# Kernel tuning notes

Measured on AMD Instinct MI355X. Metric: run time of the kernel, lower is better.

The kernel has to match this reference:

```python
import jax, jax.numpy as jnp
import numpy as np

B, N, D, H = 4, 2048, 1024, 16
HD = D // H
SCALE = D ** -0.5  # NOTE: original scales by dimension**-0.5 (not head_dim**-0.5)


def setup_inputs() -> dict:
    key = jax.random.key(0)
    k1, k2, k3 = jax.random.split(key, 3)
    x = jax.random.normal(k1, (B, N, D), dtype=jnp.float32)
    w_qkv = jax.random.normal(k2, (D, 3 * D), dtype=jnp.float32) * (D ** -0.5)
    w_proj = jax.random.normal(k3, (D, D), dtype=jnp.float32) * (D ** -0.5)
    b_proj = jnp.zeros((D,), dtype=jnp.float32)
    return {"x": x, "w_qkv": w_qkv, "w_proj": w_proj, "b_proj": b_proj}


def reference(x, w_qkv, w_proj, b_proj):
    # qkv projection: [B,N,3D] -> split into q,k,v each [B,H,N,HD]
    qkv = x @ w_qkv
    qkv = qkv.reshape(B, N, 3, H, HD).transpose(2, 0, 3, 1, 4)  # [3,B,H,N,HD]
    q, k, v = qkv[0], qkv[1], qkv[2]
    scores = jnp.einsum('bhid,bhjd->bhij', q, k) * SCALE
    attn = jax.nn.softmax(scores, axis=-1)
    out = jnp.einsum('bhij,bhjd->bhid', attn, v)  # [B,H,N,HD]
    out = out.transpose(0, 2, 1, 3).reshape(B, N, D)
    return out @ w_proj + b_proj
```

## Files before the change

### kernel.cpp

```cpp
#include <hip/hip_runtime.h>
#include <stdint.h>

#define Bdim 4
#define Nseq 2048
#define Dmod 1024
#define Hn   16
#define HD   64
#define SCALE 0.03125f
#define L2E   1.44269504089f

typedef __attribute__((ext_vector_type(8))) short short8;
typedef __attribute__((ext_vector_type(8))) unsigned short ushort8;
typedef __attribute__((ext_vector_type(4))) float f32x4;
typedef __attribute__((ext_vector_type(16))) float f32x16;

typedef __attribute__((address_space(3))) uint32_t lds_u32;
typedef __attribute__((address_space(1))) const uint32_t glob_u32;

static __device__ __forceinline__ void gload_lds16(const unsigned short* g, unsigned short* l) {
    __builtin_amdgcn_global_load_lds((glob_u32*)(const void*)g, (lds_u32*)(void*)l, 16, 0, 0);
}

static __device__ __forceinline__ unsigned short f2bf(float f) {
    union { float f; uint32_t u; } v; v.f = f;
    uint32_t r = (v.u + 0x7FFFu + ((v.u >> 16) & 1u)) >> 16;
    return (unsigned short)r;
}

__global__ __launch_bounds__(256) void cast_x_kernel(const float* __restrict__ in,
                                                     unsigned short* __restrict__ out, int n4) {
    int i = blockIdx.x * blockDim.x + threadIdx.x;
    int stride = gridDim.x * blockDim.x;
    for (; i < n4; i += stride) {
        float4 v = reinterpret_cast<const float4*>(in)[i];
        ushort4 o;
        o.x = f2bf(v.x); o.y = f2bf(v.y); o.z = f2bf(v.z); o.w = f2bf(v.w);
        reinterpret_cast<ushort4*>(out)[i] = o;
    }
}

__global__ void transpose_cast_kernel(const float* __restrict__ in,
                                      unsigned short* __restrict__ out, int R, int C) {
    __shared__ unsigned short t[32][33];
    int c0 = blockIdx.x * 32, r0 = blockIdx.y * 32;
    int tx = threadIdx.x, ty = threadIdx.y;
#pragma unroll
    for (int i = 0; i < 4; ++i)
        t[ty + i*8][tx] = f2bf(in[(size_t)(r0 + ty + i*8) * C + c0 + tx]);
    __syncthreads();
#pragma unroll
    for (int i = 0; i < 4; ++i)
        out[(size_t)(c0 + ty + i*8) * R + r0 + tx] = t[tx][ty + i*8];
}

template<bool OUT_BF16, bool BIAS, bool VSPLIT>
__global__ __launch_bounds__(256) void gemm_bt_kernel(const unsigned short* __restrict__ A,
                                                      const unsigned short* __restrict__ Bt,
                                                      void* __restrict__ Cv,
                                                      const float* __restrict__ bias,
                                                      unsigned short* __restrict__ vTp,
                                                      int M, int N, int K) {
    __shared__ unsigned short Al[128 * 64];
    __shared__ unsigned short Bl[128 * 64];
    int tid = threadIdx.x;
    int lane = tid & 63, wv = tid >> 6;
    int wr = (wv >> 1) * 64, wc = (wv & 1) * 64;
    int lr = lane & 15, lg = lane >> 4, lk = lg * 8;

    int gx = gridDim.x;
    int lin = blockIdx.y * gx + blockIdx.x;
    int cpx = (gx * gridDim.y) >> 3;
    int nl = (lin & 7) * cpx + (lin >> 3);
    int m0 = (nl / gx) * 128, n0 = (nl % gx) * 128;

    int srow = wv * 8 + (lane >> 3);
    int scol = (lane & 7) * 8;
    const unsigned short* ag = A  + (size_t)(m0 + srow) * K + scol;
    const unsigned short* bg = Bt + (size_t)(n0 + srow) * K + scol;
    unsigned short* la = Al + wv * 512;
    unsigned short* lb = Bl + wv * 512;

    f32x4 acc[4][4];
#pragma unroll
    for (int i = 0; i < 4; ++i)
#pragma unroll
        for (int j = 0; j < 4; ++j) acc[i][j] = (f32x4)0.f;

    for (int k0 = 0; k0 < K; k0 += 64) {
        __syncthreads();
#pragma unroll
        for (int i = 0; i < 4; ++i) {
            gload_lds16(ag + (size_t)i * 32 * K + k0, la + i * 2048);
            gload_lds16(bg + (size_t)i * 32 * K + k0, lb + i * 2048);
        }
        __syncthreads();
#pragma unroll
        for (int ks = 0; ks < 2; ++ks) {
            short8 a[4], b[4];
#pragma unroll
            for (int mi = 0; mi < 4; ++mi)
                a[mi] = *reinterpret_cast<const short8*>(Al + (wr + mi*16 + lr) * 64 + ks*32 + lk);
#pragma unroll
            for (int nj = 0; nj < 4; ++nj)
                b[nj] = *reinterpret_cast<const short8*>(Bl + (wc + nj*16 + lr) * 64 + ks*32 + lk);
#pragma unroll
            for (int mi = 0; mi < 4; ++mi)
#pragma unroll
                for (int nj = 0; nj < 4; ++nj)
                    acc[mi][nj] = __builtin_amdgcn_mfma_f32_16x16x32_bf16(a[mi], b[nj], acc[mi][nj], 0, 0, 0);
        }
    }
#pragma unroll
    for (int mi = 0; mi < 4; ++mi) {
#pragma unroll
        for (int nj = 0; nj < 4; ++nj) {
            int r = m0 + wr + mi*16 + lg*4;
            int c = n0 + wc + nj*16 + lr;
            if (VSPLIT && c >= 2048) {
                int cc = c - 2048;
                int bh = ((r >> 11) << 4) + (cc >> 6);
                int d = cc & 63;
                ushort4 o4;
                o4.x = f2bf(acc[mi][nj][0]);
                o4.y = f2bf(acc[mi][nj][1]);
                o4.z = f2bf(acc[mi][nj][2]);
                o4.w = f2bf(acc[mi][nj][3]);
                *reinterpret_cast<ushort4*>(vTp + ((size_t)(bh * 64 + d) * 2048) + (r & 2047)) = o4;
            } else {
                float bv = BIAS ? bias[c] : 0.f;
#pragma unroll
                for (int i = 0; i < 4; ++i) {
                    float v = acc[mi][nj][i] + bv;
                    if (OUT_BF16)
                        reinterpret_cast<unsigned short*>(Cv)[(size_t)(r + i) * N + c] = f2bf(v);
                    else
                        reinterpret_cast<float*>(Cv)[(size_t)(r + i) * N + c] = v;
                }
            }
        }
    }
}

__global__ __launch_bounds__(256, 2) void attn_kernel(const unsigned short* __restrict__ qkv,
                                                      const unsigned short* __restrict__ vT,
                                                      unsigned short* __restrict__ attn_o) {
    __shared__ unsigned short Kl[2 * 64 * 64];
    __shared__ unsigned short Vl[2 * 64 * 64];

    int w = blockIdx.x;
    int lid = (w & 7) * 64 + (w >> 3);
    int bh = lid >> 3, qb = lid & 7;
    int b = bh >> 4, h = bh & 15;

    int tid = threadIdx.x, lane = tid & 63, wv = tid >> 6;
    int lr = lane & 31, hi = lane >> 5;
    int q0 = qb * 256 + wv * 64;

    short8 qfA[4], qfB[4];
    {
        const unsigned short* qrowA = qkv + (size_t)(b * Nseq + q0 + lr) * 3072 + h * 64 + hi * 8;
        const unsigned short* qrowB = qrowA + (size_t)32 * 3072;
#pragma unroll
        for (int ks = 0; ks < 4; ++ks) {
            qfA[ks] = *reinterpret_cast<const short8*>(qrowA + ks * 16);
            qfB[ks] = *reinterpret_cast<const short8*>(qrowB + ks * 16);
        }
    }

    float mrunA = -1e30f, lrunA = 0.f, mrunB = -1e30f, lrunB = 0.f;
    f32x16 oA0 = (f32x16)0.f, oA1 = (f32x16)0.f, oB0 = (f32x16)0.f, oB1 = (f32x16)0.f;

    int sr = tid >> 2;
    const unsigned short* kg = qkv + (size_t)(b * Nseq + sr) * 3072 + 1024 + h * 64 + (tid & 3) * 16;
    const unsigned short* vg = vT + ((size_t)(bh * 64 + sr)) * Nseq + (tid & 3) * 16;
    int sb = (sr >> 5) * 4096 + (tid & 3) * 1024 + (sr & 31) * 16;

    {
        ushort8 a0 = *reinterpret_cast<const ushort8*>(kg);
        ushort8 a1 = *reinterpret_cast<const ushort8*>(kg + 8);
        ushort8 a2 = *reinterpret_cast<const ushort8*>(vg);
        ushort8 a3 = *reinterpret_cast<const ushort8*>(vg + 8);
        *reinterpret_cast<ushort8*>((char*)Kl + sb) = a0;
        *reinterpret_cast<ushort8*>((char*)Kl + sb + 512) = a1;
        *reinterpret_cast<ushort8*>((char*)Vl + sb) = a2;
        *reinterpret_cast<ushort8*>((char*)Vl + sb + 512) = a3;
    }
    ushort8 k0r = *reinterpret_cast<const ushort8*>(kg + (size_t)64 * 3072);
    ushort8 k1r = *reinterpret_cast<const ushort8*>(kg + (size_t)64 * 3072 + 8);
    ushort8 v0r = *reinterpret_cast<const ushort8*>(vg + 64);
    ushort8 v1r = *reinterpret_cast<const ushort8*>(vg + 72);

    int cur = 0;
    for (int jt = 0; jt < Nseq; jt += 64, cur ^= 1) {
        __syncthreads();
        int rb = cur * 8192, wb = rb ^ 8192;

        f32x16 sA0 = (f32x16)0.f, sA1 = (f32x16)0.f, sB0 = (f32x16)0.f, sB1 = (f32x16)0.f;
        __builtin_amdgcn_s_setprio(1);
#pragma unroll
        for (int ks = 0; ks < 4; ++ks) {
            short8 kf0 = *reinterpret_cast<const short8*>((char*)Kl + rb + ks*1024 + lane*16);
            short8 kf1 = *reinterpret_cast<const short8*>((char*)Kl + rb + 4096 + ks*1024 + lane*16);
            sA0 = __builtin_amdgcn_mfma_f32_32x32x16_bf16(kf0, qfA[ks], sA0, 0, 0, 0);
            sA1 = __builtin_amdgcn_mfma_f32_32x32x16_bf16(kf1, qfA[ks], sA1, 0, 0, 0);
            sB0 = __builtin_amdgcn_mfma_f32_32x32x16_bf16(kf0, qfB[ks], sB0, 0, 0, 0);
            sB1 = __builtin_amdgcn_mfma_f32_32x32x16_bf16(kf1, qfB[ks], sB1, 0, 0, 0);
        }
        __builtin_amdgcn_s_setprio(0);

        if (jt + 64 < Nseq) {
            *reinterpret_cast<ushort8*>((char*)Kl + wb + sb) = k0r;
            *reinterpret_cast<ushort8*>((char*)Kl + wb + sb + 512) = k1r;
            *reinterpret_cast<ushort8*>((char*)Vl + wb + sb) = v0r;
            *reinterpret_cast<ushort8*>((char*)Vl + wb + sb + 512) = v1r;
            int jn = jt + 128;
            if (jn < Nseq) {
                k0r = *reinterpret_cast<const ushort8*>(kg + (size_t)jn * 3072);
                k1r = *reinterpret_cast<const ushort8*>(kg + (size_t)jn * 3072 + 8);
                v0r = *reinterpret_cast<const ushort8*>(vg + jn);
                v1r = *reinterpret_cast<const ushort8*>(vg + jn + 8);
            }
        }

        float tA[16], tB[16];
#pragma unroll
        for (int i = 0; i < 16; ++i) { tA[i] = fmaxf(sA0[i], sA1[i]); tB[i] = fmaxf(sB0[i], sB1[i]); }
#pragma unroll
        for (int st = 8; st > 0; st >>= 1)
#pragma unroll
            for (int i = 0; i < st; ++i) { tA[i] = fmaxf(tA[i], tA[i + st]); tB[i] = fmaxf(tB[i], tB[i + st]); }
        float mlocA = fmaxf(tA[0], __shfl_xor(tA[0], 32)) * SCALE;
        float mlocB = fmaxf(tB[0], __shfl_xor(tB[0], 32)) * SCALE;

        if (!__all((mlocA <= mrunA + 8.f) && (mlocB <= mrunB + 8.f))) {
            float mnA = fmaxf(mrunA, mlocA);
            float fA = __builtin_amdgcn_exp2f((mrunA - mnA) * L2E);
            float mnB = fmaxf(mrunB, mlocB);
            float fB = __builtin_amdgcn_exp2f((mrunB - mnB) * L2E);
            lrunA *= fA; lrunB *= fB; mrunA = mnA; mrunB = mnB;
#pragma unroll
            for (int i = 0; i < 16; ++i) {
                oA0[i] *= fA; oA1[i] *= fA; oB0[i] *= fB; oB1[i] *= fB;
            }
        }

        const float c1 = SCALE * L2E;
        float c0A = -mrunA * L2E, c0B = -mrunB * L2E;
        float pA0[16], pA1[16], pB0[16], pB1[16];
#pragma unroll
        for (int i = 0; i < 16; ++i) {
            pA0[i] = __builtin_amdgcn_exp2f(fmaf(sA0[i], c1, c0A));
            pA1[i] = __builtin_amdgcn_exp2f(fmaf(sA1[i], c1, c0A));
            pB0[i] = __builtin_amdgcn_exp2f(fmaf(sB0[i], c1, c0B));
            pB1[i] = __builtin_amdgcn_exp2f(fmaf(sB1[i], c1, c0B));
        }

        float aA[16], aB[16];
#pragma unroll
        for (int i = 0; i < 16; ++i) { aA[i] = pA0[i] + pA1[i]; aB[i] = pB0[i] + pB1[i]; }
#pragma unroll
        for (int st = 8; st > 0; st >>= 1)
#pragma unroll
            for (int i = 0; i < st; ++i) { aA[i] += aA[i + st]; aB[i] += aB[i + st]; }
        lrunA += aA[0] + __shfl_xor(aA[0], 32);
        lrunB += aB[0] + __shfl_xor(aB[0], 32);

        uint32_t UA[16], UB[16];
#pragma unroll
        for (int m = 0; m < 8; ++m) {
            asm("v_cvt_pk_bf16_f32 %0, %1, %2" : "=v"(UA[m])   : "v"(pA0[2*m]), "v"(pA0[2*m+1]));
            asm("v_cvt_pk_bf16_f32 %0, %1, %2" : "=v"(UA[8+m]) : "v"(pA1[2*m]), "v"(pA1[2*m+1]));
            asm("v_cvt_pk_bf16_f32 %0, %1, %2" : "=v"(UB[m])   : "v"(pB0[2*m]), "v"(pB0[2*m+1]));
            asm("v_cvt_pk_bf16_f32 %0, %1, %2" : "=v"(UB[8+m]) : "v"(pB1[2*m]), "v"(pB1[2*m+1]));
        }
        uint32_t rvA[8], rvB[8];
#pragma unroll
        for (int g = 0; g < 2; ++g) {
            const int o = g * 8, ro = g * 4;
            rvA[ro+0] = (uint32_t)__shfl_xor((int)(hi ? UA[o+0] : UA[o+2]), 32);
            rvA[ro+1] = (uint32_t)__shfl_xor((int)(hi ? UA[o+1] : UA[o+3]), 32);
            rvA[ro+2] = (uint32_t)__shfl_xor((int)(hi ? UA[o+4] : UA[o+6]), 32);
            rvA[ro+3] = (uint32_t)__shfl_xor((int)(hi ? UA[o+5] : UA[o+7]), 32);
            rvB[ro+0] = (uint32_t)__shfl_xor((int)(hi ? UB[o+0] : UB[o+2]), 32);
            rvB[ro+1] = (uint32_t)__shfl_xor((int)(hi ? UB[o+1] : UB[o+3]), 32);
            rvB[ro+2] = (uint32_t)__shfl_xor((int)(hi ? UB[o+4] : UB[o+6]), 32);
            rvB[ro+3] = (uint32_t)__shfl_xor((int)(hi ? UB[o+5] : UB[o+7]), 32);
        }

        __builtin_amdgcn_s_setprio(1);
#pragma unroll
        for (int ks4 = 0; ks4 < 4; ++ks4) {
            const int hh = 8*(ks4>>1) + 4*(ks4&1);
            const int rc = 4*(ks4>>1) + 2*(ks4&1);
            union { uint32_t u[4]; short8 s; } fA, fB;
            fA.u[0] = hi ? rvA[rc]    : UA[hh];
            fA.u[1] = hi ? rvA[rc+1]  : UA[hh+1];
            fA.u[2] = hi ? UA[hh+2]   : rvA[rc];
            fA.u[3] = hi ? UA[hh+3]   : rvA[rc+1];
            fB.u[0] = hi ? rvB[rc]    : UB[hh];
            fB.u[1] = hi ? rvB[rc+1]  : UB[hh+1];
            fB.u[2] = hi ? UB[hh+2]   : rvB[rc];
            fB.u[3] = hi ? UB[hh+3]   : rvB[rc+1];
            short8 vf0 = *reinterpret_cast<const short8*>((char*)Vl + rb + ks4*1024 + lane*16);
            short8 vf1 = *reinterpret_cast<const short8*>((char*)Vl + rb + 4096 + ks4*1024 + lane*16);
            oA0 = __builtin_amdgcn_mfma_f32_32x32x16_bf16(vf0, fA.s, oA0, 0, 0, 0);
            oA1 = __builtin_amdgcn_mfma_f32_32x32x16_bf16(vf1, fA.s, oA1, 0, 0, 0);
            oB0 = __builtin_amdgcn_mfma_f32_32x32x16_bf16(vf0, fB.s, oB0, 0, 0, 0);
            oB1 = __builtin_amdgcn_mfma_f32_32x32x16_bf16(vf1, fB.s, oB1, 0, 0, 0);
        }
        __builtin_amdgcn_s_setprio(0);
    }

    float invA = 1.f / lrunA, invB = 1.f / lrunB;
    unsigned short* orowA = attn_o + (size_t)(b * Nseq + q0 + lr) * Dmod + h * 64;
    unsigned short* orowB = attn_o + (size_t)(b * Nseq + q0 + 32 + lr) * Dmod + h * 64;
#pragma unroll
    for (int db = 0; db < 2; ++db)
#pragma unroll
        for (int g = 0; g < 4; ++g) {
            int d = db * 32 + 8 * g + 4 * hi;
            ushort4 o4;
            o4.x = f2bf((db ? oA1[4*g+0] : oA0[4*g+0]) * invA);
            o4.y = f2bf((db ? oA1[4*g+1] : oA0[4*g+1]) * invA);
            o4.z = f2bf((db ? oA1[4*g+2] : oA0[4*g+2]) * invA);
            o4.w = f2bf((db ? oA1[4*g+3] : oA0[4*g+3]) * invA);
            *reinterpret_cast<ushort4*>(orowA + d) = o4;
            o4.x = f2bf((db ? oB1[4*g+0] : oB0[4*g+0]) * invB);
            o4.y = f2bf((db ? oB1[4*g+1] : oB0[4*g+1]) * invB);
            o4.z = f2bf((db ? oB1[4*g+2] : oB0[4*g+2]) * invB);
            o4.w = f2bf((db ? oB1[4*g+3] : oB0[4*g+3]) * invB);
            *reinterpret_cast<ushort4*>(orowB + d) = o4;
        }
}

extern "C" void kernel_launch(void* const* d_in, const int* in_sizes, int n_in,
                              void* d_out, int out_size, void* d_ws, size_t ws_size,
                              hipStream_t stream) {
    const float* x      = (const float*)d_in[0];
    const float* w_qkv  = (const float*)d_in[1];
    const float* w_proj = (const float*)d_in[2];
    const float* b_proj = (const float*)d_in[3];
    float* out = (float*)d_out;
    char* ws = (char*)d_ws;

    unsigned short* qkv    = (unsigned short*)(ws);
    unsigned short* vT     = (unsigned short*)(ws + 50331648);
    unsigned short* xb     = (unsigned short*)(ws + 67108864);
    unsigned short* attn_o = xb;
    unsigned short* wqkvT  = (unsigned short*)(ws + 83886080);
    unsigned short* wprojT = (unsigned short*)(ws + 90177536);

    cast_x_kernel<<<2048, 256, 0, stream>>>(x, xb, (Bdim*Nseq*Dmod)/4);
    transpose_cast_kernel<<<dim3(3072/32, 1024/32), dim3(32, 8), 0, stream>>>(w_qkv, wqkvT, 1024, 3072);
    transpose_cast_kernel<<<dim3(1024/32, 1024/32), dim3(32, 8), 0, stream>>>(w_proj, wprojT, 1024, 1024);
    gemm_bt_kernel<true, false, true><<<dim3(3072/128, 8192/128), 256, 0, stream>>>(
        xb, wqkvT, qkv, nullptr, vT, Bdim*Nseq, 3*Dmod, Dmod);
    attn_kernel<<<512, 256, 0, stream>>>(qkv, vT, attn_o);
    gemm_bt_kernel<false, true, false><<<dim3(1024/128, 8192/128), 256, 0, stream>>>(
        attn_o, wprojT, out, b_proj, nullptr, Bdim*Nseq, Dmod, Dmod);
}
```

Baseline: 226.8 us.

## Software-pipeline QK^T one tile ahead and load K/V via direct global-to-LDS copies

Restructures the attention loop so the QK^T MFMAs for the next KV tile are issued while softmax and PV for the current tile run, using ping-pong score accumulators. K/V tiles are now fetched with global_load_lds straight into LDS instead of staged through registers, and V moves to a triple buffer so the prefetch can stay in flight across the extra pipeline stage. The goal is to hide softmax VALU latency behind matrix work and cut register staging and load latency. In exchange it uses more registers for the second set of score accumulators and more LDS, which could lower occupancy.

```diff
diff --git a/kernel.cpp b/kernel.cpp
--- a/kernel.cpp
+++ b/kernel.cpp
@@ -145,7 +145,7 @@
                                                       const unsigned short* __restrict__ vT,
                                                       unsigned short* __restrict__ attn_o) {
     __shared__ unsigned short Kl[2 * 64 * 64];
-    __shared__ unsigned short Vl[2 * 64 * 64];
+    __shared__ unsigned short Vl[3 * 64 * 64];
 
     int w = blockIdx.x;
     int lid = (w & 7) * 64 + (w >> 3);
@@ -170,61 +170,66 @@
     float mrunA = -1e30f, lrunA = 0.f, mrunB = -1e30f, lrunB = 0.f;
     f32x16 oA0 = (f32x16)0.f, oA1 = (f32x16)0.f, oB0 = (f32x16)0.f, oB1 = (f32x16)0.f;
 
-    int sr = tid >> 2;
-    const unsigned short* kg = qkv + (size_t)(b * Nseq + sr) * 3072 + 1024 + h * 64 + (tid & 3) * 16;
-    const unsigned short* vg = vT + ((size_t)(bh * 64 + sr)) * Nseq + (tid & 3) * 16;
-    int sb = (sr >> 5) * 4096 + (tid & 3) * 1024 + (sr & 31) * 16;
-
-    {
-        ushort8 a0 = *reinterpret_cast<const ushort8*>(kg);
-        ushort8 a1 = *reinterpret_cast<const ushort8*>(kg + 8);
-        ushort8 a2 = *reinterpret_cast<const ushort8*>(vg);
-        ushort8 a3 = *reinterpret_cast<const ushort8*>(vg + 8);
-        *reinterpret_cast<ushort8*>((char*)Kl + sb) = a0;
-        *reinterpret_cast<ushort8*>((char*)Kl + sb + 512) = a1;
-        *reinterpret_cast<ushort8*>((char*)Vl + sb) = a2;
-        *reinterpret_cast<ushort8*>((char*)Vl + sb + 512) = a3;
-    }
-    ushort8 k0r = *reinterpret_cast<const ushort8*>(kg + (size_t)64 * 3072);
-    ushort8 k1r = *reinterpret_cast<const ushort8*>(kg + (size_t)64 * 3072 + 8);
-    ushort8 v0r = *reinterpret_cast<const ushort8*>(vg + 64);
-    ushort8 v1r = *reinterpret_cast<const ushort8*>(vg + 72);
-
-    int cur = 0;
-    for (int jt = 0; jt < Nseq; jt += 64, cur ^= 1) {
+    int c0 = wv * 128 + lane, c1 = c0 + 64;
+    int kv0 = ((c0 >> 8) << 5) + (c0 & 31), d00 = (((c0 >> 6) & 3) << 4) + (((c0 >> 5) & 1) << 3);
+    int kv1 = ((c1 >> 8) << 5) + (c1 & 31), d01 = (((c1 >> 6) & 3) << 4) + (((c1 >> 5) & 1) << 3);
+    const unsigned short* kp0 = qkv + (size_t)(b * Nseq + kv0) * 3072 + 1024 + h * 64 + d00;
+    const unsigned short* kp1 = qkv + (size_t)(b * Nseq + kv1) * 3072 + 1024 + h * 64 + d01;
+    const unsigned short* vp0 = vT + ((size_t)(bh * 64 + kv0)) * Nseq + d00;
+    const unsigned short* vp1 = vT + ((size_t)(bh * 64 + kv1)) * Nseq + d01;
+    unsigned short* kld = (unsigned short*)((char*)Kl + wv * 2048);
+    unsigned short* vld = (unsigned short*)((char*)Vl + wv * 2048);
+
+    gload_lds16(kp0, kld);            gload_lds16(kp1, kld + 512);
+    gload_lds16(vp0, vld);            gload_lds16(vp1, vld + 512);
+    kp0 += 64 * 3072; kp1 += 64 * 3072; vp0 += 64; vp1 += 64;
+    gload_lds16(kp0, kld + 4096);     gload_lds16(kp1, kld + 4096 + 512);
+    gload_lds16(vp0, vld + 4096);     gload_lds16(vp1, vld + 4096 + 512);
+    kp0 += 64 * 3072; kp1 += 64 * 3072; vp0 += 64; vp1 += 64;
+    __syncthreads();
+
+    f32x16 xA0, xA1, xB0, xB1, yA0, yA1, yB0, yB1;
+    xA0 = (f32x16)0.f; xA1 = (f32x16)0.f; xB0 = (f32x16)0.f; xB1 = (f32x16)0.f;
+#pragma unroll
+    for (int ks = 0; ks < 4; ++ks) {
+        short8 kf0 = *reinterpret_cast<const short8*>((char*)Kl + ks*1024 + lane*16);
+        short8 kf1 = *reinterpret_cast<const short8*>((char*)Kl + 4096 + ks*1024 + lane*16);
+        xA0 = __builtin_amdgcn_mfma_f32_32x32x16_bf16(kf0, qfA[ks], xA0, 0, 0, 0);
+        xA1 = __builtin_amdgcn_mfma_f32_32x32x16_bf16(kf1, qfA[ks], xA1, 0, 0, 0);
+        xB0 = __builtin_amdgcn_mfma_f32_32x32x16_bf16(kf0, qfB[ks], xB0, 0, 0, 0);
+        xB1 = __builtin_amdgcn_mfma_f32_32x32x16_bf16(kf1, qfB[ks], xB1, 0, 0, 0);
+    }
+
+    auto tile_body = [&](f32x16& SA0, f32x16& SA1, f32x16& SB0, f32x16& SB1,
+                         f32x16& NA0, f32x16& NA1, f32x16& NB0, f32x16& NB1,
+                         int t, int vro, int vwo) {
         __syncthreads();
-        int rb = cur * 8192, wb = rb ^ 8192;
-
-        f32x16 sA0 = (f32x16)0.f, sA1 = (f32x16)0.f, sB0 = (f32x16)0.f, sB1 = (f32x16)0.f;
-        __builtin_amdgcn_s_setprio(1);
-#pragma unroll
-        for (int ks = 0; ks < 4; ++ks) {
-            short8 kf0 = *reinterpret_cast<const short8*>((char*)Kl + rb + ks*1024 + lane*16);
-            short8 kf1 = *reinterpret_cast<const short8*>((char*)Kl + rb + 4096 + ks*1024 + lane*16);
-            sA0 = __builtin_amdgcn_mfma_f32_32x32x16_bf16(kf0, qfA[ks], sA0, 0, 0, 0);
-            sA1 = __builtin_amdgcn_mfma_f32_32x32x16_bf16(kf1, qfA[ks], sA1, 0, 0, 0);
-            sB0 = __builtin_amdgcn_mfma_f32_32x32x16_bf16(kf0, qfB[ks], sB0, 0, 0, 0);
-            sB1 = __builtin_amdgcn_mfma_f32_32x32x16_bf16(kf1, qfB[ks], sB1, 0, 0, 0);
-        }
-        __builtin_amdgcn_s_setprio(0);
-
-        if (jt + 64 < Nseq) {
-            *reinterpret_cast<ushort8*>((char*)Kl + wb + sb) = k0r;
-            *reinterpret_cast<ushort8*>((char*)Kl + wb + sb + 512) = k1r;
-            *reinterpret_cast<ushort8*>((char*)Vl + wb + sb) = v0r;
-            *reinterpret_cast<ushort8*>((char*)Vl + wb + sb + 512) = v1r;
-            int jn = jt + 128;
-            if (jn < Nseq) {
-                k0r = *reinterpret_cast<const ushort8*>(kg + (size_t)jn * 3072);
-                k1r = *reinterpret_cast<const ushort8*>(kg + (size_t)jn * 3072 + 8);
-                v0r = *reinterpret_cast<const ushort8*>(vg + jn);
-                v1r = *reinterpret_cast<const ushort8*>(vg + jn + 8);
+
+        if (t < 30) {
+            unsigned short* kd = (unsigned short*)((char*)Kl + (t & 1) * 8192 + wv * 2048);
+            unsigned short* vd = (unsigned short*)((char*)Vl + vwo + wv * 2048);
+            gload_lds16(kp0, kd);       gload_lds16(kp1, kd + 512);
+            gload_lds16(vp0, vd);       gload_lds16(vp1, vd + 512);
+            kp0 += 64 * 3072; kp1 += 64 * 3072; vp0 += 64; vp1 += 64;
+        }
+
+        if (t < 31) {
+            char* kb = (char*)Kl + ((t + 1) & 1) * 8192;
+            NA0 = (f32x16)0.f; NA1 = (f32x16)0.f; NB0 = (f32x16)0.f; NB1 = (f32x16)0.f;
+#pragma unroll
+            for (int ks = 0; ks < 4; ++ks) {
+                short8 kf0 = *reinterpret_cast<const short8*>(kb + ks*1024 + lane*16);
+                short8 kf1 = *reinterpret_cast<const short8*>(kb + 4096 + ks*1024 + lane*16);
+                NA0 = __builtin_amdgcn_mfma_f32_32x32x16_bf16(kf0, qfA[ks], NA0, 0, 0, 0);
+                NA1 = __builtin_amdgcn_mfma_f32_32x32x16_bf16(kf1, qfA[ks], NA1, 0, 0, 0);
+                NB0 = __builtin_amdgcn_mfma_f32_32x32x16_bf16(kf0, qfB[ks], NB0, 0, 0, 0);
+                NB1 = __builtin_amdgcn_mfma_f32_32x32x16_bf16(kf1, qfB[ks], NB1, 0, 0, 0);
             }
         }
 
         float tA[16], tB[16];
 #pragma unroll
-        for (int i = 0; i < 16; ++i) { tA[i] = fmaxf(sA0[i], sA1[i]); tB[i] = fmaxf(sB0[i], sB1[i]); }
+        for (int i = 0; i < 16; ++i) { tA[i] = fmaxf(SA0[i], SA1[i]); tB[i] = fmaxf(SB0[i], SB1[i]); }
 #pragma unroll
         for (int st = 8; st > 0; st >>= 1)
 #pragma unroll
@@ -244,20 +249,19 @@
             }
         }
 
-        const float c1 = SCALE * L2E;
+        const float c1f = SCALE * L2E;
         float c0A = -mrunA * L2E, c0B = -mrunB * L2E;
-        float pA0[16], pA1[16], pB0[16], pB1[16];
 #pragma unroll
         for (int i = 0; i < 16; ++i) {
-            pA0[i] = __builtin_amdgcn_exp2f(fmaf(sA0[i], c1, c0A));
-            pA1[i] = __builtin_amdgcn_exp2f(fmaf(sA1[i], c1, c0A));
-            pB0[i] = __builtin_amdgcn_exp2f(fmaf(sB0[i], c1, c0B));
-            pB1[i] = __builtin_amdgcn_exp2f(fmaf(sB1[i], c1, c0B));
+            SA0[i] = __builtin_amdgcn_exp2f(fmaf(SA0[i], c1f, c0A));
+            SA1[i] = __builtin_amdgcn_exp2f(fmaf(SA1[i], c1f, c0A));
+            SB0[i] = __builtin_amdgcn_exp2f(fmaf(SB0[i], c1f, c0B));
+            SB1[i] = __builtin_amdgcn_exp2f(fmaf(SB1[i], c1f, c0B));
         }
 
         float aA[16], aB[16];
 #pragma unroll
-        for (int i = 0; i < 16; ++i) { aA[i] = pA0[i] + pA1[i]; aB[i] = pB0[i] + pB1[i]; }
+        for (int i = 0; i < 16; ++i) { aA[i] = SA0[i] + SA1[i]; aB[i] = SB0[i] + SB1[i]; }
 #pragma unroll
         for (int st = 8; st > 0; st >>= 1)
 #pragma unroll
@@ -268,10 +272,10 @@
         uint32_t UA[16], UB[16];
 #pragma unroll
         for (int m = 0; m < 8; ++m) {
-            asm("v_cvt_pk_bf16_f32 %0, %1, %2" : "=v"(UA[m])   : "v"(pA0[2*m]), "v"(pA0[2*m+1]));
-            asm("v_cvt_pk_bf16_f32 %0, %1, %2" : "=v"(UA[8+m]) : "v"(pA1[2*m]), "v"(pA1[2*m+1]));
-            asm("v_cvt_pk_bf16_f32 %0, %1, %2" : "=v"(UB[m])   : "v"(pB0[2*m]), "v"(pB0[2*m+1]));
-            asm("v_cvt_pk_bf16_f32 %0, %1, %2" : "=v"(UB[8+m]) : "v"(pB1[2*m]), "v"(pB1[2*m+1]));
+            asm("v_cvt_pk_bf16_f32 %0, %1, %2" : "=v"(UA[m])   : "v"(SA0[2*m]), "v"(SA0[2*m+1]));
+            asm("v_cvt_pk_bf16_f32 %0, %1, %2" : "=v"(UA[8+m]) : "v"(SA1[2*m]), "v"(SA1[2*m+1]));
+            asm("v_cvt_pk_bf16_f32 %0, %1, %2" : "=v"(UB[m])   : "v"(SB0[2*m]), "v"(SB0[2*m+1]));
+            asm("v_cvt_pk_bf16_f32 %0, %1, %2" : "=v"(UB[8+m]) : "v"(SB1[2*m]), "v"(SB1[2*m+1]));
         }
         uint32_t rvA[8], rvB[8];
 #pragma unroll
@@ -287,6 +291,7 @@
             rvB[ro+3] = (uint32_t)__shfl_xor((int)(hi ? UB[o+5] : UB[o+7]), 32);
         }
 
+        char* vb = (char*)Vl + vro;
         __builtin_amdgcn_s_setprio(1);
 #pragma unroll
         for (int ks4 = 0; ks4 < 4; ++ks4) {
@@ -301,14 +306,24 @@
             fB.u[1] = hi ? rvB[rc+1]  : UB[hh+1];
             fB.u[2] = hi ? UB[hh+2]   : rvB[rc];
             fB.u[3] = hi ? UB[hh+3]   : rvB[rc+1];
-            short8 vf0 = *reinterpret_cast<const short8*>((char*)Vl + rb + ks4*1024 + lane*16);
-            short8 vf1 = *reinterpret_cast<const short8*>((char*)Vl + rb + 4096 + ks4*1024 + lane*16);
+            short8 vf0 = *reinterpret_cast<const short8*>(vb + ks4*1024 + lane*16);
+            short8 vf1 = *reinterpret_cast<const short8*>(vb + 4096 + ks4*1024 + lane*16);
             oA0 = __builtin_amdgcn_mfma_f32_32x32x16_bf16(vf0, fA.s, oA0, 0, 0, 0);
             oA1 = __builtin_amdgcn_mfma_f32_32x32x16_bf16(vf1, fA.s, oA1, 0, 0, 0);
             oB0 = __builtin_amdgcn_mfma_f32_32x32x16_bf16(vf0, fB.s, oB0, 0, 0, 0);
             oB1 = __builtin_amdgcn_mfma_f32_32x32x16_bf16(vf1, fB.s, oB1, 0, 0, 0);
         }
         __builtin_amdgcn_s_setprio(0);
+    };
+
+    int vro = 0, vwo = 16384;
+    for (int t = 0; t < 32; t += 2) {
+        tile_body(xA0, xA1, xB0, xB1, yA0, yA1, yB0, yB1, t, vro, vwo);
+        vro = (vro == 16384) ? 0 : vro + 8192;
+        vwo = (vwo == 16384) ? 0 : vwo + 8192;
+        tile_body(yA0, yA1, yB0, yB1, xA0, xA1, xB0, xB1, t + 1, vro, vwo);
+        vro = (vro == 16384) ? 0 : vro + 8192;
+        vwo = (vwo == 16384) ? 0 : vwo + 8192;
     }
 
     float invA = 1.f / lrunA, invB = 1.f / lrunB;
```

Result: slower. 284.9 us (+25.6%).
